# Optimization experiments

Measured on AMD Instinct MI355X. Metric: run time of the kernel, lower is better.

Reference implementation:

```python
import jax, jax.numpy as jnp
import numpy as np

B, CIN, COUT, T, K = 8, 64, 64, 16384, 127


def setup_inputs() -> dict:
    key = jax.random.key(0)
    kx, kw = jax.random.split(key)
    x = jax.random.normal(kx, (B, CIN, T), dtype=jnp.float32)
    sigma = np.sqrt(2.0 / (CIN * K + COUT)).astype(np.float32)
    W = jax.random.normal(kw, (COUT, CIN, K), dtype=jnp.float32) * sigma
    return {"x": x, "W": W}


def reference(x, W):
    # Full linear convolution via FFT (true convolution, matches
    # torchaudio.functional.fftconvolve), summed over in_channels,
    # then trimmed to mode='same' (output length == T, centered).
    T_ = x.shape[-1]
    K_ = W.shape[-1]
    n = T_ + K_ - 1  # linear-conv length, no circular wraparound
    Xf = jnp.fft.rfft(x, n=n)   # [B, Cin, nf] complex
    Wf = jnp.fft.rfft(W, n=n)   # [Cout, Cin, nf] complex
    # Batched complex multiply-accumulate over in_channels (single pass,
    # no per-output-channel redundant FFTs).
    Yf = jnp.einsum('bif,oif->bof', Xf, Wf)  # [B, Cout, nf]
    y_full = jnp.fft.irfft(Yf, n=n)          # [B, Cout, T+K-1]
    start = (K_ - 1) // 2                    # 'same': centered crop
    return y_full[..., start:start + T_]
```

## Files before the change

### kernel.cpp

```cpp
#include <hip/hip_runtime.h>

#define T_LEN 16384
#define CIN   64
#define COUT  64
#define KTAPS 127
#define TN    256
#define XROWS 384
#define XPITCH_B 144
#define WT_KS 4096

typedef __attribute__((ext_vector_type(8)))  __bf16 bf16x8;
typedef __attribute__((ext_vector_type(16))) float  f32x16;
typedef __attribute__((ext_vector_type(4)))  float  float4v;

__device__ inline unsigned short f2bf(float f) {
    unsigned u = __builtin_bit_cast(unsigned, f);
    u += 0x7fffu + ((u >> 16) & 1u);
    return (unsigned short)(u >> 16);
}

__global__ void wt_transform(const float* __restrict__ W,
                             unsigned short* __restrict__ Wt) {
    int t  = blockIdx.x * 256 + threadIdx.x;
    int kp = t >> 9, c = t & 511;
    int f = c >> 6, kg = (c >> 5) & 1, l31 = c & 31;
    int cc = f >> 1, m = f & 1;
    int o = m * 32 + l31, ib = cc * 16 + kg * 8;
    const float* src = W + (o * CIN + ib) * KTAPS + (126 - kp);
    unsigned short tmp[8];
    #pragma unroll
    for (int e = 0; e < 8; ++e)
        tmp[e] = f2bf(src[e * KTAPS]);
    uint4 pk;
    pk.x = (unsigned)tmp[0] | ((unsigned)tmp[1] << 16);
    pk.y = (unsigned)tmp[2] | ((unsigned)tmp[3] << 16);
    pk.z = (unsigned)tmp[4] | ((unsigned)tmp[5] << 16);
    pk.w = (unsigned)tmp[6] | ((unsigned)tmp[7] << 16);
    *(uint4*)(Wt + kp * WT_KS + c * 8) = pk;
}

__global__ __launch_bounds__(256, 2)
void conv_mfma(const float* __restrict__ x,
               const unsigned short* __restrict__ Wt,
               float* __restrict__ y) {
    __shared__ __align__(16) char pool[XROWS * XPITCH_B];
    unsigned short* xs = (unsigned short*)pool;

    const int tid = threadIdx.x;
    const int bb  = blockIdx.x >> 6;
    const int tt  = blockIdx.x & 63;
    const int t0  = tt * TN;

    {
        const int cin = tid >> 2;
        const int s   = tid & 3;
        const float* xrow = x + (bb * CIN + cin) * T_LEN;
        for (int j = 0; j < 24; ++j) {
            const int w = 16 * j + 4 * s;
            const int u = t0 - 64 + w;
            float4v v;
            if (u >= 0 && u + 4 <= T_LEN) {
                v = *(const float4v*)(xrow + u);
            } else {
                v.x = (u + 0 >= 0 && u + 0 < T_LEN) ? xrow[u + 0] : 0.f;
                v.y = (u + 1 >= 0 && u + 1 < T_LEN) ? xrow[u + 1] : 0.f;
                v.z = (u + 2 >= 0 && u + 2 < T_LEN) ? xrow[u + 2] : 0.f;
                v.w = (u + 3 >= 0 && u + 3 < T_LEN) ? xrow[u + 3] : 0.f;
            }
            #pragma unroll
            for (int e = 0; e < 4; ++e) {
                const int we = w + e;
                const float fv = (e == 0) ? v.x : (e == 1) ? v.y : (e == 2) ? v.z : v.w;
                xs[we * 72 + cin] = f2bf(fv);
            }
        }
    }

    const int lane   = tid & 63;
    const int wv     = tid >> 6;
    const int quad   = wv >> 1;
    const int ww     = wv & 1;
    const int l31    = lane & 31;
    const int kg     = lane >> 5;
    const int twbase = ww * 128;
    const int brow0  = twbase + l31 + 1;

    const int kp0  = quad ? 64 : 0;
    const int ntap = quad ? 63 : 64;

    const char* ab = (const char*)Wt + lane * 16;

    f32x16 acc[2][4] = {};
    uint4 a0r[8], a1r[8];
    uint4 bA[4], bB[4];

    #define LOADA(dst, kp)                                                  \
        do { const char* p_ = ab + (kp) * 8192;                             \
            _Pragma("unroll")                                               \
            for (int f = 0; f < 8; ++f)                                     \
                dst[f] = *(const uint4*)(p_ + f * 1024); } while (0)

    #define LOADB(dst, rb, cidx)                                            \
        do { const char* xp_ = (const char*)xs + (rb) * XPITCH_B            \
                               + ((2 * (cidx) + kg) << 4);                  \
            _Pragma("unroll")                                               \
            for (int n = 0; n < 4; ++n)                                     \
                dst[n] = *(const uint4*)(xp_ + n * (32 * XPITCH_B));        \
        } while (0)

    #define MFMAB(bv, ar, cidx)                                             \
        do { bf16x8 a0 = __builtin_bit_cast(bf16x8, ar[(cidx) * 2 + 0]);    \
            bf16x8 a1 = __builtin_bit_cast(bf16x8, ar[(cidx) * 2 + 1]);     \
            _Pragma("unroll")                                               \
            for (int n = 0; n < 4; ++n) {                                   \
                bf16x8 b = __builtin_bit_cast(bf16x8, bv[n]);               \
                acc[0][n] = __builtin_amdgcn_mfma_f32_32x32x16_bf16(a0, b, acc[0][n], 0, 0, 0); \
                acc[1][n] = __builtin_amdgcn_mfma_f32_32x32x16_bf16(a1, b, acc[1][n], 0, 0, 0); \
            } } while (0)

    #define TAP(ar, kp)                                                     \
        do {                                                                \
            LOADB(bB, brow0 + (kp), 1);     MFMAB(bA, ar, 0);               \
            LOADB(bA, brow0 + (kp), 2);     MFMAB(bB, ar, 1);               \
            LOADB(bB, brow0 + (kp), 3);     MFMAB(bA, ar, 2);               \
            LOADB(bA, brow0 + (kp) + 1, 0); MFMAB(bB, ar, 3);               \
        } while (0)

    LOADA(a0r, kp0);
    __syncthreads();

    for (int z = 0; z < wv; ++z)
        __builtin_amdgcn_s_sleep(2);

    LOADB(bA, brow0 + kp0, 0);

    for (int i = 0; i < ntap; i += 2) {
        if (i + 1 < ntap) LOADA(a1r, kp0 + i + 1);
        TAP(a0r, kp0 + i);
        if (i + 2 < ntap) LOADA(a0r, kp0 + i + 2);
        if (i + 1 < ntap) TAP(a1r, kp0 + i + 1);
    }

    __syncthreads();
    float* msm = (float*)pool;
    #pragma unroll
    for (int m = 0; m < 2; ++m) {
        if (quad == 1) {
            #pragma unroll
            for (int n = 0; n < 4; ++n)
                #pragma unroll
                for (int r = 0; r < 16; ++r)
                    msm[(n * 16 + r) * 128 + ww * 64 + lane] = acc[m][n][r];
        }
        __syncthreads();
        if (quad == 0) {
            #pragma unroll
            for (int n = 0; n < 4; ++n)
                #pragma unroll
                for (int r = 0; r < 16; ++r)
                    acc[m][n][r] += msm[(n * 16 + r) * 128 + ww * 64 + lane];
        }
        __syncthreads();
    }

    if (quad == 0) {
        const int ybase = (bb * COUT) * T_LEN;
        #pragma unroll
        for (int m = 0; m < 2; ++m) {
            #pragma unroll
            for (int n = 0; n < 4; ++n) {
                const int t = t0 + twbase + n * 32 + l31;
                #pragma unroll
                for (int r = 0; r < 16; ++r) {
                    const int o = m * 32 + (r & 3) + 8 * (r >> 2) + 4 * kg;
                    y[ybase + o * T_LEN + t] = acc[m][n][r];
                }
            }
        }
    }
}

extern "C" void kernel_launch(void* const* d_in, const int* in_sizes, int n_in,
                              void* d_out, int out_size, void* d_ws, size_t ws_size,
                              hipStream_t stream) {
    const float* x = (const float*)d_in[0];
    const float* W = (const float*)d_in[1];
    float* yout = (float*)d_out;
    unsigned short* Wt = (unsigned short*)d_ws;

    wt_transform<<<(KTAPS * 512) / 256, 256, 0, stream>>>(W, Wt);

    const int grid = 8 * (T_LEN / TN);
    conv_mfma<<<grid, 256, 0, stream>>>(x, Wt, yout);
}
```

Measured before the change: 116.4 us.

## Reuse shared-memory B fragments across four taps by grouping taps in strides of 32

Pads the weight transform to 128 taps, with a zero tap, so the tap range splits evenly. The main loop now handles taps jj, jj+32, jj+64 and jj+96 together. It loads seven shared-memory row fragments per channel chunk and reuses overlapping fragments across the four taps, which cuts LDS reads per MFMA. In exchange it drops the software-pipelined double-buffered A prefetch: weights are now loaded from global or L2 right before use. It also adds work for one all-zero padded tap.

```diff
diff --git a/kernel.cpp b/kernel.cpp
--- a/kernel.cpp
+++ b/kernel.cpp
@@ -23,19 +23,21 @@
                              unsigned short* __restrict__ Wt) {
     int t  = blockIdx.x * 256 + threadIdx.x;
     int kp = t >> 9, c = t & 511;
-    int f = c >> 6, kg = (c >> 5) & 1, l31 = c & 31;
-    int cc = f >> 1, m = f & 1;
-    int o = m * 32 + l31, ib = cc * 16 + kg * 8;
-    const float* src = W + (o * CIN + ib) * KTAPS + (126 - kp);
-    unsigned short tmp[8];
-    #pragma unroll
-    for (int e = 0; e < 8; ++e)
-        tmp[e] = f2bf(src[e * KTAPS]);
-    uint4 pk;
-    pk.x = (unsigned)tmp[0] | ((unsigned)tmp[1] << 16);
-    pk.y = (unsigned)tmp[2] | ((unsigned)tmp[3] << 16);
-    pk.z = (unsigned)tmp[4] | ((unsigned)tmp[5] << 16);
-    pk.w = (unsigned)tmp[6] | ((unsigned)tmp[7] << 16);
+    uint4 pk = {0, 0, 0, 0};
+    if (kp < KTAPS) {
+        int f = c >> 6, kg = (c >> 5) & 1, l31 = c & 31;
+        int cc = f >> 1, m = f & 1;
+        int o = m * 32 + l31, ib = cc * 16 + kg * 8;
+        const float* src = W + (o * CIN + ib) * KTAPS + (126 - kp);
+        unsigned short tmp[8];
+        #pragma unroll
+        for (int e = 0; e < 8; ++e)
+            tmp[e] = f2bf(src[e * KTAPS]);
+        pk.x = (unsigned)tmp[0] | ((unsigned)tmp[1] << 16);
+        pk.y = (unsigned)tmp[2] | ((unsigned)tmp[3] << 16);
+        pk.z = (unsigned)tmp[4] | ((unsigned)tmp[5] << 16);
+        pk.w = (unsigned)tmp[6] | ((unsigned)tmp[7] << 16);
+    }
     *(uint4*)(Wt + kp * WT_KS + c * 8) = pk;
 }
 
@@ -84,61 +86,68 @@
     const int kg     = lane >> 5;
     const int twbase = ww * 128;
     const int brow0  = twbase + l31 + 1;
-
-    const int kp0  = quad ? 64 : 0;
-    const int ntap = quad ? 63 : 64;
-
-    const char* ab = (const char*)Wt + lane * 16;
+    const int j0     = quad ? 16 : 0;
 
     f32x16 acc[2][4] = {};
-    uint4 a0r[8], a1r[8];
-    uint4 bA[4], bB[4];
-
-    #define LOADA(dst, kp)                                                  \
-        do { const char* p_ = ab + (kp) * 8192;                             \
-            _Pragma("unroll")                                               \
-            for (int f = 0; f < 8; ++f)                                     \
-                dst[f] = *(const uint4*)(p_ + f * 1024); } while (0)
-
-    #define LOADB(dst, rb, cidx)                                            \
-        do { const char* xp_ = (const char*)xs + (rb) * XPITCH_B            \
-                               + ((2 * (cidx) + kg) << 4);                  \
-            _Pragma("unroll")                                               \
-            for (int n = 0; n < 4; ++n)                                     \
-                dst[n] = *(const uint4*)(xp_ + n * (32 * XPITCH_B));        \
-        } while (0)
-
-    #define MFMAB(bv, ar, cidx)                                             \
-        do { bf16x8 a0 = __builtin_bit_cast(bf16x8, ar[(cidx) * 2 + 0]);    \
-            bf16x8 a1 = __builtin_bit_cast(bf16x8, ar[(cidx) * 2 + 1]);     \
-            _Pragma("unroll")                                               \
-            for (int n = 0; n < 4; ++n) {                                   \
-                bf16x8 b = __builtin_bit_cast(bf16x8, bv[n]);               \
-                acc[0][n] = __builtin_amdgcn_mfma_f32_32x32x16_bf16(a0, b, acc[0][n], 0, 0, 0); \
-                acc[1][n] = __builtin_amdgcn_mfma_f32_32x32x16_bf16(a1, b, acc[1][n], 0, 0, 0); \
-            } } while (0)
-
-    #define TAP(ar, kp)                                                     \
-        do {                                                                \
-            LOADB(bB, brow0 + (kp), 1);     MFMAB(bA, ar, 0);               \
-            LOADB(bA, brow0 + (kp), 2);     MFMAB(bB, ar, 1);               \
-            LOADB(bB, brow0 + (kp), 3);     MFMAB(bA, ar, 2);               \
-            LOADB(bA, brow0 + (kp) + 1, 0); MFMAB(bB, ar, 3);               \
-        } while (0)
-
-    LOADA(a0r, kp0);
+
     __syncthreads();
 
     for (int z = 0; z < wv; ++z)
         __builtin_amdgcn_s_sleep(2);
 
-    LOADB(bA, brow0 + kp0, 0);
-
-    for (int i = 0; i < ntap; i += 2) {
-        if (i + 1 < ntap) LOADA(a1r, kp0 + i + 1);
-        TAP(a0r, kp0 + i);
-        if (i + 2 < ntap) LOADA(a0r, kp0 + i + 2);
-        if (i + 1 < ntap) TAP(a1r, kp0 + i + 1);
+    const char* xsb = (const char*)xs;
+    const char* wtb = (const char*)Wt + (unsigned)lane * 16;
+
+    for (int j = 0; j < 16; ++j) {
+        const int jj = j0 + j;
+        const int rb = brow0 + jj;
+        const char* arow = wtb + jj * 8192;
+        #pragma unroll
+        for (int cc = 0; cc < 4; ++cc) {
+            uint4 F[7];
+            const char* xp = xsb + rb * XPITCH_B + ((2 * cc + kg) << 4);
+            #pragma unroll
+            for (int p = 0; p < 7; ++p)
+                F[p] = *(const uint4*)(xp + p * (32 * XPITCH_B));
+            {
+                uint4 a00 = *(const uint4*)(arow +            (cc * 2 + 0) * 1024);
+                uint4 a01 = *(const uint4*)(arow +            (cc * 2 + 1) * 1024);
+                uint4 a10 = *(const uint4*)(arow + 262144 +   (cc * 2 + 0) * 1024);
+                uint4 a11 = *(const uint4*)(arow + 262144 +   (cc * 2 + 1) * 1024);
+                #pragma unroll
+                for (int n = 0; n < 4; ++n) {
+                    bf16x8 b0 = __builtin_bit_cast(bf16x8, F[n]);
+                    acc[0][n] = __builtin_amdgcn_mfma_f32_32x32x16_bf16(
+                        __builtin_bit_cast(bf16x8, a00), b0, acc[0][n], 0, 0, 0);
+                    acc[1][n] = __builtin_amdgcn_mfma_f32_32x32x16_bf16(
+                        __builtin_bit_cast(bf16x8, a01), b0, acc[1][n], 0, 0, 0);
+                    bf16x8 b1 = __builtin_bit_cast(bf16x8, F[n + 1]);
+                    acc[0][n] = __builtin_amdgcn_mfma_f32_32x32x16_bf16(
+                        __builtin_bit_cast(bf16x8, a10), b1, acc[0][n], 0, 0, 0);
+                    acc[1][n] = __builtin_amdgcn_mfma_f32_32x32x16_bf16(
+                        __builtin_bit_cast(bf16x8, a11), b1, acc[1][n], 0, 0, 0);
+                }
+            }
+            {
+                uint4 a20 = *(const uint4*)(arow + 524288 +   (cc * 2 + 0) * 1024);
+                uint4 a21 = *(const uint4*)(arow + 524288 +   (cc * 2 + 1) * 1024);
+                uint4 a30 = *(const uint4*)(arow + 786432 +   (cc * 2 + 0) * 1024);
+                uint4 a31 = *(const uint4*)(arow + 786432 +   (cc * 2 + 1) * 1024);
+                #pragma unroll
+                for (int n = 0; n < 4; ++n) {
+                    bf16x8 b2 = __builtin_bit_cast(bf16x8, F[n + 2]);
+                    acc[0][n] = __builtin_amdgcn_mfma_f32_32x32x16_bf16(
+                        __builtin_bit_cast(bf16x8, a20), b2, acc[0][n], 0, 0, 0);
+                    acc[1][n] = __builtin_amdgcn_mfma_f32_32x32x16_bf16(
+                        __builtin_bit_cast(bf16x8, a21), b2, acc[1][n], 0, 0, 0);
+                    bf16x8 b3 = __builtin_bit_cast(bf16x8, F[n + 3]);
+                    acc[0][n] = __builtin_amdgcn_mfma_f32_32x32x16_bf16(
+                        __builtin_bit_cast(bf16x8, a30), b3, acc[0][n], 0, 0, 0);
+                    acc[1][n] = __builtin_amdgcn_mfma_f32_32x32x16_bf16(
+                        __builtin_bit_cast(bf16x8, a31), b3, acc[1][n], 0, 0, 0);
+                }
+            }
+        }
     }
 
     __syncthreads();
@@ -188,7 +197,7 @@
     float* yout = (float*)d_out;
     unsigned short* Wt = (unsigned short*)d_ws;
 
-    wt_transform<<<(KTAPS * 512) / 256, 256, 0, stream>>>(W, Wt);
+    wt_transform<<<(128 * 512) / 256, 256, 0, stream>>>(W, Wt);
 
     const int grid = 8 * (T_LEN / TN);
     conv_mfma<<<grid, 256, 0, stream>>>(x, Wt, yout);
```

New measurement: 119.1 us. 1.02x slower.
